# Performance work log

Measured on AMD Instinct MI355X. Metric: run time of the kernel, lower is better.

## Reference

```python
import jax, jax.numpy as jnp
import numpy as np

N, E, D = 50000, 800000, 128
EPS_BN = 1e-5   # torch BatchNorm1d default eps
EPS_AGG = 1e-6  # aggregation denominator eps


def setup_inputs() -> dict:
    key = jax.random.key(0)
    ks = jax.random.split(key, 20)
    s = 1.0 / np.sqrt(D)
    inp = {
        'h': jax.random.normal(ks[0], (N, D), jnp.float32),
        'e': jax.random.normal(ks[1], (E, D), jnp.float32),
    }
    for i, name in enumerate(['A1', 'A2', 'A3', 'B1', 'B2', 'B3']):
        inp['W_' + name] = (jax.random.normal(ks[2 + i], (D, D), jnp.float32) * s)
        inp['b_' + name] = (jax.random.normal(ks[8 + i], (D,), jnp.float32) * s)
    inp['gamma_e'] = jnp.ones((D,), jnp.float32)
    inp['beta_e'] = jnp.zeros((D,), jnp.float32)
    inp['gamma_h'] = jnp.ones((D,), jnp.float32)
    inp['beta_h'] = jnp.zeros((D,), jnp.float32)
    inp['src'] = jax.random.randint(ks[14], (E,), 0, N, dtype=jnp.int32)
    inp['dst'] = jax.random.randint(ks[15], (E,), 0, N, dtype=jnp.int32)
    return inp


def _bn(x, gamma, beta):
    # BatchNorm1d in training mode: biased batch statistics per channel
    mu = jnp.mean(x, axis=0)
    var = jnp.var(x, axis=0)
    return (x - mu) * jax.lax.rsqrt(var + EPS_BN) * gamma + beta


def reference(h, e, W_A1, b_A1, W_A2, b_A2, W_A3, b_A3,
              W_B1, b_B1, W_B2, b_B2, W_B3, b_B3,
              gamma_e, beta_e, gamma_h, beta_h, src, dst):
    n = h.shape[0]
    A1h = h @ W_A1 + b_A1
    A2h = h @ W_A2 + b_A2
    A3h = h @ W_A3 + b_A3
    B1h = h @ W_B1 + b_B1
    B2h = h @ W_B2 + b_B2
    B3e = e @ W_B3 + b_B3

    # Edge gate: e_ji (forward graph) == e_ik (reverse graph) by construction
    e_pre = B1h[src] + B2h[dst] + B3e            # [E, D]
    e_act = jax.nn.relu(_bn(e_pre, gamma_e, beta_e)) + e  # residual
    sigma = jax.nn.sigmoid(e_act)                # [E, D]

    seg = lambda v, idx: jax.ops.segment_sum(v, idx, num_segments=n)
    # forward aggregation at dst, backward aggregation (reverse graph) at src
    h_fwd = seg(sigma * A2h[src], dst) / (seg(sigma, dst) + EPS_AGG)
    h_bwd = seg(sigma * A3h[dst], src) / (seg(sigma, src) + EPS_AGG)

    h_new = A1h + h_fwd + h_bwd
    h_out = jax.nn.relu(_bn(h_new, gamma_h, beta_h)) + h  # residual; dropout p=0
    return h_out
```

## Files before the change

### kernel.cpp

```cpp
#include <hip/hip_runtime.h>
#include <hip/hip_bf16.h>

#define N_NODES 50000
#define N_EDGES 800000
#define D 128
#define NODE_TILES 3125
#define EDGE_TILES 50000

typedef __attribute__((ext_vector_type(4))) float f32x4;
typedef __attribute__((ext_vector_type(2))) float f32x2;
typedef __attribute__((ext_vector_type(8))) short bf16x8;

__device__ __forceinline__ unsigned short f2bf(float f) {
    __hip_bfloat16 h = __float2bfloat16(f);
    return __builtin_bit_cast(unsigned short, h);
}
__device__ __forceinline__ float bf2f(short s) {
    return __builtin_bit_cast(float, ((unsigned)(unsigned short)s) << 16);
}
__device__ __forceinline__ float bflo(unsigned u) { return __builtin_bit_cast(float, u << 16); }
__device__ __forceinline__ float bfhi(unsigned u) { return __builtin_bit_cast(float, u & 0xffff0000u); }

struct WPtrs   { const float* p[6]; };
struct NodeArgs{ const float* bias[3]; unsigned short* out[3]; int widx[3]; };


__global__ __launch_bounds__(256) void k_prep(WPtrs wp, unsigned short* __restrict__ wfrag) {
    int idx = blockIdx.x * 256 + threadIdx.x;
    if (idx >= 6 * 16384) return;
    int w  = idx >> 14;
    int r  = idx & 16383;
    int j  = r & 7;
    int l  = (r >> 3) & 63;
    int kc = r >> 9;
    int ki = kc >> 3, ct = kc & 7;
    int k  = ki * 32 + ((l >> 4) << 3) + j;
    int c  = ct * 16 + (l & 15);
    wfrag[idx] = f2bf(wp.p[w][k * D + c]);
}

__global__ __launch_bounds__(256) void k_node_gemm(const float* __restrict__ x,
                                                   const unsigned short* __restrict__ wfrag,
                                                   NodeArgs na, int ntiles) {
    __shared__ unsigned short ldsw[16384];
    const int z = blockIdx.z;
    {
        const uint4* sp = (const uint4*)(wfrag + (size_t)na.widx[z] * 16384);
        uint4* dp = (uint4*)ldsw;
        for (int i = threadIdx.x; i < 2048; i += 256) dp[i] = sp[i];
    }
    __syncthreads();
    const int lane = threadIdx.x & 63, wave = threadIdx.x >> 6;
    const int tile = blockIdx.x * 4 + wave;
    if (tile >= ntiles) return;
    const int lrow = lane & 15, lgrp = lane >> 4;

    const float* bias = na.bias[z];
    float bias_r[8];
#pragma unroll
    for (int ct = 0; ct < 8; ct++) bias_r[ct] = bias[ct * 16 + lrow];

    f32x4 acc[8];
#pragma unroll
    for (int ct = 0; ct < 8; ct++) acc[ct] = (f32x4)0.0f;

    const float* arow = x + (size_t)(tile * 16 + lrow) * D + lgrp * 8;
#pragma unroll
    for (int ki = 0; ki < 4; ki++) {
        f32x4 a0 = *(const f32x4*)(arow + ki * 32);
        f32x4 a1 = *(const f32x4*)(arow + ki * 32 + 4);
        bf16x8 af;
#pragma unroll
        for (int q = 0; q < 4; q++) { af[q] = (short)f2bf(a0[q]); af[q + 4] = (short)f2bf(a1[q]); }
#pragma unroll
        for (int ct = 0; ct < 8; ct++) {
            bf16x8 bf = *(const bf16x8*)(ldsw + ((ki * 8 + ct) * 64 + lane) * 8);
            acc[ct] = __builtin_amdgcn_mfma_f32_16x16x32_bf16(af, bf, acc[ct], 0, 0, 0);
        }
    }
    unsigned short* out16 = na.out[z];
#pragma unroll
    for (int j = 0; j < 4; j++) {
        bf16x8 pk;
#pragma unroll
        for (int ct = 0; ct < 8; ct++) pk[ct] = (short)f2bf(acc[ct][j] + bias_r[ct]);
        int rr = tile * 16 + lgrp * 4 + j;
        *(bf16x8*)(out16 + (size_t)rr * 128 + lrow * 8) = pk;
    }
}

__global__ __launch_bounds__(256) void k_hist(const int* __restrict__ src, const int* __restrict__ dst,
                                              int* __restrict__ cnt_f, int* __restrict__ cnt_b) {
    int e = blockIdx.x * 256 + threadIdx.x;
    if (e < N_EDGES) {
        atomicAdd(&cnt_f[dst[e]], 1);
        atomicAdd(&cnt_b[src[e]], 1);
    }
}

__global__ __launch_bounds__(1024) void k_scan(const int* __restrict__ cntf, int* __restrict__ offf,
                                               const int* __restrict__ cntb, int* __restrict__ offb) {
    const int* cnt = blockIdx.x ? cntb : cntf;
    int* off = blockIdx.x ? offb : offf;
    const int CH = 49;
    int t = threadIdx.x;
    int base = t * CH;
    int s = 0;
    for (int j = 0; j < CH; j++) { int i = base + j; s += (i < N_NODES) ? cnt[i] : 0; }
    __shared__ int tot[1024];
    tot[t] = s;
    __syncthreads();
    for (int d = 1; d < 1024; d <<= 1) {
        int v = (t >= d) ? tot[t - d] : 0;
        __syncthreads();
        tot[t] += v;
        __syncthreads();
    }
    int run = tot[t] - s;
    for (int j = 0; j < CH; j++) {
        int i = base + j;
        if (i < N_NODES) { run += cnt[i]; off[i + 1] = run; }
    }
    if (t == 0) off[0] = 0;
}

__global__ __launch_bounds__(256) void k_rank(const int* __restrict__ src, const int* __restrict__ dst,
                                              const int* __restrict__ off_f, const int* __restrict__ off_b,
                                              int* __restrict__ cnt2_f, int* __restrict__ cnt2_b,
                                              int2* __restrict__ idx_f, int2* __restrict__ idx_b) {
    int e = blockIdx.x * 256 + threadIdx.x;
    if (e < N_EDGES) {
        int d = dst[e], s = src[e];
        int rf = atomicAdd(&cnt2_f[d], 1);
        idx_f[off_f[d] + rf] = make_int2(e, s);
        int rb = atomicAdd(&cnt2_b[s], 1);
        idx_b[off_b[s] + rb] = make_int2(e, d);
    }
}

__global__ __launch_bounds__(256) void k_gather_stats(
        unsigned short* __restrict__ epre16,
        const unsigned short* __restrict__ B1p, const unsigned short* __restrict__ B2p,
        const int* __restrict__ src, const int* __restrict__ dst,
        float* __restrict__ ssum, float* __restrict__ sssq) {
    const int lane = threadIdx.x & 63, wave = threadIdx.x >> 6;
    const int t = lane & 15, sub = lane >> 4;
    float ss[8] = {0,0,0,0,0,0,0,0}, sq[8] = {0,0,0,0,0,0,0,0};
    const int NP = N_EDGES / 8;
    for (int q = blockIdx.x * 4 + wave; q < NP; q += gridDim.x * 4) {
        const int r0 = q * 8 + sub;
        const int r1 = r0 + 4;
        const int s0 = src[r0], d0 = dst[r0];
        const int s1 = src[r1], d1 = dst[r1];
        bf16x8 p0  = *(const bf16x8*)(epre16 + (((size_t)r0) << 7) + t * 8);
        bf16x8 p1  = *(const bf16x8*)(epre16 + (((size_t)r1) << 7) + t * 8);
        bf16x8 g1a = *(const bf16x8*)(B1p + (size_t)s0 * 128 + t * 8);
        bf16x8 g2a = *(const bf16x8*)(B2p + (size_t)d0 * 128 + t * 8);
        bf16x8 g1b = *(const bf16x8*)(B1p + (size_t)s1 * 128 + t * 8);
        bf16x8 g2b = *(const bf16x8*)(B2p + (size_t)d1 * 128 + t * 8);
        bf16x8 o0, o1;
#pragma unroll
        for (int ct = 0; ct < 8; ct++) {
            float v0 = bf2f(p0[ct]) + bf2f(g1a[ct]) + bf2f(g2a[ct]);
            float v1 = bf2f(p1[ct]) + bf2f(g1b[ct]) + bf2f(g2b[ct]);
            o0[ct] = (short)f2bf(v0);
            o1[ct] = (short)f2bf(v1);
            ss[ct] += v0 + v1; sq[ct] += v0 * v0 + v1 * v1;
        }
        *(bf16x8*)(epre16 + (((size_t)r0) << 7) + t * 8) = o0;
        *(bf16x8*)(epre16 + (((size_t)r1) << 7) + t * 8) = o1;
    }
#pragma unroll
    for (int ct = 0; ct < 8; ct++) {
        float a = ss[ct], b = sq[ct];
        a += __shfl_xor(a, 16); a += __shfl_xor(a, 32);
        b += __shfl_xor(b, 16); b += __shfl_xor(b, 32);
        if (lane < 16) {
            atomicAdd(&ssum[ct * 16 + lane], a);
            atomicAdd(&sssq[ct * 16 + lane], b);
        }
    }
}

__global__ void k_bnparam(const float* __restrict__ ssum, const float* __restrict__ sssq,
                          const float* __restrict__ gamma, const float* __restrict__ beta,
                          float cnt, float* __restrict__ scale, float* __restrict__ shift) {
    int c = threadIdx.x;
    float mu  = ssum[c] / cnt;
    float var = sssq[c] / cnt - mu * mu;
    float rs  = rsqrtf(var + 1e-5f);
    float sc  = rs * gamma[c];
    scale[c] = sc;
    shift[c] = beta[c] - mu * sc;
}

__global__ __launch_bounds__(256) void k_sigma(const float* __restrict__ e,
        const unsigned short* __restrict__ epre16, unsigned char* __restrict__ sigma,
        const float* __restrict__ scale_e, const float* __restrict__ shift_e) {
    const int lane = threadIdx.x & 63, wave = threadIdx.x >> 6;
    const int t = lane & 15, sub = lane >> 4;
    float sc[8], sh[8];
#pragma unroll
    for (int ct = 0; ct < 8; ct++) {
        int ch = ct * 16 + t;
        sc[ct] = scale_e[ch]; sh[ct] = shift_e[ch];
    }
    const int NQ = N_EDGES / 4;
    for (int q = blockIdx.x * 4 + wave; q < NQ; q += gridDim.x * 4) {
        const int r = q * 4 + sub;
        bf16x8 pk = *(const bf16x8*)(epre16 + (((size_t)r) << 7) + t * 8);
        const float* er = e + (size_t)r * 128 + t;
        float sg[8];
#pragma unroll
        for (int ct = 0; ct < 8; ct++) {
            float xn = bf2f(pk[ct]) * sc[ct] + sh[ct];
            float ea = fmaxf(xn, 0.0f) + er[ct * 16];
            sg[ct] = 1.0f / (1.0f + __expf(-ea));
        }
        int lo = 0, hi = 0;
        lo = __builtin_amdgcn_cvt_pk_fp8_f32(sg[0], sg[1], lo, false);
        lo = __builtin_amdgcn_cvt_pk_fp8_f32(sg[2], sg[3], lo, true);
        hi = __builtin_amdgcn_cvt_pk_fp8_f32(sg[4], sg[5], hi, false);
        hi = __builtin_amdgcn_cvt_pk_fp8_f32(sg[6], sg[7], hi, true);
        uint2 v; v.x = (unsigned)lo; v.y = (unsigned)hi;
        *(uint2*)(sigma + (size_t)r * 128 + t * 8) = v;
    }
}

__global__ __launch_bounds__(256) void k_aggregate(
        const unsigned char* __restrict__ sigma,
        const unsigned short* __restrict__ A1p, const unsigned short* __restrict__ A2p,
        const unsigned short* __restrict__ A3p,
        const int* __restrict__ off_f, const int2* __restrict__ idx_f,
        const int* __restrict__ off_b, const int2* __restrict__ idx_b,
        float* __restrict__ hnewp, float* __restrict__ ssum, float* __restrict__ sssq) {
    const int lane = threadIdx.x & 63, wave = threadIdx.x >> 6;
    const int wgl = blockIdx.x * 4 + wave;
    float ps0 = 0, pq0 = 0, ps1 = 0, pq1 = 0;
#pragma unroll 1
    for (int n = wgl * 4; n < wgl * 4 + 4; n++) {
        float fn0 = 0, fd0 = 0, fn1 = 0, fd1 = 0;
        float bn0 = 0, bd0 = 0, bn1 = 0, bd1 = 0;
        {
            int beg = off_f[n], end = off_f[n + 1];
            int i = beg;
            for (; i + 4 <= end; i += 4) {
                int2 e0 = idx_f[i], e1 = idx_f[i + 1], e2 = idx_f[i + 2], e3 = idx_f[i + 3];
                unsigned short w0 = *(const unsigned short*)(sigma + (size_t)e0.x * 128 + 2 * lane);
                unsigned short w1 = *(const unsigned short*)(sigma + (size_t)e1.x * 128 + 2 * lane);
                unsigned short w2 = *(const unsigned short*)(sigma + (size_t)e2.x * 128 + 2 * lane);
                unsigned short w3 = *(const unsigned short*)(sigma + (size_t)e3.x * 128 + 2 * lane);
                unsigned a0 = *(const unsigned*)(A2p + (size_t)e0.y * 128 + 2 * lane);
                unsigned a1 = *(const unsigned*)(A2p + (size_t)e1.y * 128 + 2 * lane);
                unsigned a2 = *(const unsigned*)(A2p + (size_t)e2.y * 128 + 2 * lane);
                unsigned a3 = *(const unsigned*)(A2p + (size_t)e3.y * 128 + 2 * lane);
                f32x2 s0 = __builtin_amdgcn_cvt_pk_f32_fp8((int)w0, false);
                f32x2 s1 = __builtin_amdgcn_cvt_pk_f32_fp8((int)w1, false);
                f32x2 s2 = __builtin_amdgcn_cvt_pk_f32_fp8((int)w2, false);
                f32x2 s3 = __builtin_amdgcn_cvt_pk_f32_fp8((int)w3, false);
                fn0 += s0.x * bflo(a0) + s1.x * bflo(a1) + s2.x * bflo(a2) + s3.x * bflo(a3);
                fd0 += s0.x + s1.x + s2.x + s3.x;
                fn1 += s0.y * bfhi(a0) + s1.y * bfhi(a1) + s2.y * bfhi(a2) + s3.y * bfhi(a3);
                fd1 += s0.y + s1.y + s2.y + s3.y;
            }
            for (; i < end; i++) {
                int2 e0 = idx_f[i];
                unsigned short w0 = *(const unsigned short*)(sigma + (size_t)e0.x * 128 + 2 * lane);
                unsigned a0 = *(const unsigned*)(A2p + (size_t)e0.y * 128 + 2 * lane);
                f32x2 s0 = __builtin_amdgcn_cvt_pk_f32_fp8((int)w0, false);
                fn0 += s0.x * bflo(a0); fd0 += s0.x;
                fn1 += s0.y * bfhi(a0); fd1 += s0.y;
            }
        }
        {
            int beg = off_b[n], end = off_b[n + 1];
            int i = beg;
            for (; i + 4 <= end; i += 4) {
                int2 e0 = idx_b[i], e1 = idx_b[i + 1], e2 = idx_b[i + 2], e3 = idx_b[i + 3];
                unsigned short w0 = *(const unsigned short*)(sigma + (size_t)e0.x * 128 + 2 * lane);
                unsigned short w1 = *(const unsigned short*)(sigma + (size_t)e1.x * 128 + 2 * lane);
                unsigned short w2 = *(const unsigned short*)(sigma + (size_t)e2.x * 128 + 2 * lane);
                unsigned short w3 = *(const unsigned short*)(sigma + (size_t)e3.x * 128 + 2 * lane);
                unsigned a0 = *(const unsigned*)(A3p + (size_t)e0.y * 128 + 2 * lane);
                unsigned a1 = *(const unsigned*)(A3p + (size_t)e1.y * 128 + 2 * lane);
                unsigned a2 = *(const unsigned*)(A3p + (size_t)e2.y * 128 + 2 * lane);
                unsigned a3 = *(const unsigned*)(A3p + (size_t)e3.y * 128 + 2 * lane);
                f32x2 s0 = __builtin_amdgcn_cvt_pk_f32_fp8((int)w0, false);
                f32x2 s1 = __builtin_amdgcn_cvt_pk_f32_fp8((int)w1, false);
                f32x2 s2 = __builtin_amdgcn_cvt_pk_f32_fp8((int)w2, false);
                f32x2 s3 = __builtin_amdgcn_cvt_pk_f32_fp8((int)w3, false);
                bn0 += s0.x * bflo(a0) + s1.x * bflo(a1) + s2.x * bflo(a2) + s3.x * bflo(a3);
                bd0 += s0.x + s1.x + s2.x + s3.x;
                bn1 += s0.y * bfhi(a0) + s1.y * bfhi(a1) + s2.y * bfhi(a2) + s3.y * bfhi(a3);
                bd1 += s0.y + s1.y + s2.y + s3.y;
            }
            for (; i < end; i++) {
                int2 e0 = idx_b[i];
                unsigned short w0 = *(const unsigned short*)(sigma + (size_t)e0.x * 128 + 2 * lane);
                unsigned a0 = *(const unsigned*)(A3p + (size_t)e0.y * 128 + 2 * lane);
                f32x2 s0 = __builtin_amdgcn_cvt_pk_f32_fp8((int)w0, false);
                bn0 += s0.x * bflo(a0); bd0 += s0.x;
                bn1 += s0.y * bfhi(a0); bd1 += s0.y;
            }
        }
        unsigned a1 = *(const unsigned*)(A1p + (size_t)n * 128 + 2 * lane);
        float hv0 = bflo(a1) + fn0 / (fd0 + 1e-6f) + bn0 / (bd0 + 1e-6f);
        float hv1 = bfhi(a1) + fn1 / (fd1 + 1e-6f) + bn1 / (bd1 + 1e-6f);
        f32x2 hv; hv.x = hv0; hv.y = hv1;
        *(f32x2*)(hnewp + (size_t)n * 128 + 2 * lane) = hv;
        ps0 += hv0; pq0 += hv0 * hv0;
        ps1 += hv1; pq1 += hv1 * hv1;
    }
    __shared__ float red[4][64][4];
    red[wave][lane][0] = ps0; red[wave][lane][1] = pq0;
    red[wave][lane][2] = ps1; red[wave][lane][3] = pq1;
    __syncthreads();
    if (threadIdx.x < 64) {
        int l = threadIdx.x;
        float s0 = 0, q0 = 0, s1 = 0, q1 = 0;
#pragma unroll
        for (int w = 0; w < 4; w++) {
            s0 += red[w][l][0]; q0 += red[w][l][1];
            s1 += red[w][l][2]; q1 += red[w][l][3];
        }
        int c0 = (((2 * l) & 7) << 4) + (l >> 2);
        atomicAdd(&ssum[c0], s0);      atomicAdd(&sssq[c0], q0);
        atomicAdd(&ssum[c0 + 16], s1); atomicAdd(&sssq[c0 + 16], q1);
    }
}

__global__ __launch_bounds__(256) void k_hout(const float* __restrict__ hnewp,
        const float* __restrict__ h, const float* __restrict__ scale,
        const float* __restrict__ shift, float* __restrict__ out) {
    __shared__ float sc[128], sh[128];
    if (threadIdx.x < 128) { sc[threadIdx.x] = scale[threadIdx.x]; sh[threadIdx.x] = shift[threadIdx.x]; }
    __syncthreads();
    const int total = N_NODES * 32;
    for (int i = blockIdx.x * blockDim.x + threadIdx.x; i < total; i += gridDim.x * blockDim.x) {
        int r = i >> 5, c4 = (i & 31) * 4;
        f32x4 hh = *(const f32x4*)(h + (size_t)r * 128 + c4);
        f32x4 o;
#pragma unroll
        for (int k = 0; k < 4; k++) {
            int ch = c4 + k;
            int p = (ch >> 4) + ((ch & 15) << 3);
            float v = hnewp[(size_t)r * 128 + p];
            o[k] = fmaxf(v * sc[ch] + sh[ch], 0.0f) + hh[k];
        }
        *(f32x4*)(out + (size_t)r * 128 + c4) = o;
    }
}

extern "C" void kernel_launch(void* const* d_in, const int* in_sizes, int n_in,
                              void* d_out, int out_size, void* d_ws, size_t ws_size,
                              hipStream_t stream) {
    const float* h = (const float*)d_in[0];
    const float* e = (const float*)d_in[1];
    const float* W[6] = {(const float*)d_in[2], (const float*)d_in[4], (const float*)d_in[6],
                         (const float*)d_in[8], (const float*)d_in[10], (const float*)d_in[12]};
    const float* b[6] = {(const float*)d_in[3], (const float*)d_in[5], (const float*)d_in[7],
                         (const float*)d_in[9], (const float*)d_in[11], (const float*)d_in[13]};
    const float* gamma_e = (const float*)d_in[14];
    const float* beta_e  = (const float*)d_in[15];
    const float* gamma_h = (const float*)d_in[16];
    const float* beta_h  = (const float*)d_in[17];
    const int* src = (const int*)d_in[18];
    const int* dst = (const int*)d_in[19];
    float* out = (float*)d_out;

    char* ws = (char*)d_ws;
    unsigned short* wfrag = (unsigned short*)(ws);
    float* scale_e = (float*)(ws + 196608);
    float* shift_e = (float*)(ws + 197120);
    float* scale_h = (float*)(ws + 197632);
    float* shift_h = (float*)(ws + 198144);
    float* ssum_e  = (float*)(ws + 198656);
    float* sssq_e  = (float*)(ws + 199168);
    float* ssum_h  = (float*)(ws + 199680);
    float* sssq_h  = (float*)(ws + 200192);
    int*   cnt_f   = (int*)(ws + 200704);
    int*   cnt_b   = (int*)(ws + 400704);
    int*   cnt2_f  = (int*)(ws + 600704);
    int*   cnt2_b  = (int*)(ws + 800704);
    int*   off_f   = (int*)(ws + 1000704);
    int*   off_b   = (int*)(ws + 1200768);
    unsigned short* slot0 = (unsigned short*)(ws + 1400832);
    unsigned short* slot1 = slot0 + 6400000;
    unsigned short* slot2 = slot1 + 6400000;
    unsigned char* sigma = (unsigned char*)(ws + 39800832);
    int2*  idx_f   = (int2*)(ws + 142200832);
    int2*  idx_b   = idx_f + N_EDGES;
    float* hnewp   = (float*)(ws + 155000832);
    unsigned short* epre16 = (unsigned short*)(ws + 180600832);

    hipMemsetAsync(ws + 198656, 0, 802048, stream);

    WPtrs wp;
    for (int i = 0; i < 6; i++) wp.p[i] = W[i];
    k_prep<<<384, 256, 0, stream>>>(wp, wfrag);

    NodeArgs nb;
    nb.bias[0] = b[3]; nb.bias[1] = b[4]; nb.bias[2] = b[4];
    nb.out[0] = slot0; nb.out[1] = slot1; nb.out[2] = slot1;
    nb.widx[0] = 3;    nb.widx[1] = 4;    nb.widx[2] = 4;
    k_node_gemm<<<dim3(782, 1, 2), 256, 0, stream>>>(h, wfrag, nb, NODE_TILES);

    k_hist<<<3125, 256, 0, stream>>>(src, dst, cnt_f, cnt_b);
    k_scan<<<2, 1024, 0, stream>>>(cnt_f, off_f, cnt_b, off_b);
    k_rank<<<3125, 256, 0, stream>>>(src, dst, off_f, off_b, cnt2_f, cnt2_b, idx_f, idx_b);

    NodeArgs ne;
    ne.bias[0] = b[5]; ne.bias[1] = b[5]; ne.bias[2] = b[5];
    ne.out[0] = epre16; ne.out[1] = epre16; ne.out[2] = epre16;
    ne.widx[0] = 5;    ne.widx[1] = 5;    ne.widx[2] = 5;
    k_node_gemm<<<dim3(12500, 1, 1), 256, 0, stream>>>(e, wfrag, ne, EDGE_TILES);

    k_gather_stats<<<2048, 256, 0, stream>>>(epre16, slot0, slot1, src, dst, ssum_e, sssq_e);
    k_bnparam<<<1, 128, 0, stream>>>(ssum_e, sssq_e, gamma_e, beta_e, (float)N_EDGES, scale_e, shift_e);
    k_sigma<<<2048, 256, 0, stream>>>(e, epre16, sigma, scale_e, shift_e);

    NodeArgs na;
    na.bias[0] = b[0]; na.bias[1] = b[1]; na.bias[2] = b[2];
    na.out[0] = slot0; na.out[1] = slot1; na.out[2] = slot2;
    na.widx[0] = 0;    na.widx[1] = 1;    na.widx[2] = 2;
    k_node_gemm<<<dim3(782, 1, 3), 256, 0, stream>>>(h, wfrag, na, NODE_TILES);

    k_aggregate<<<3125, 256, 0, stream>>>(sigma, slot0, slot1, slot2,
                                          off_f, idx_f, off_b, idx_b, hnewp, ssum_h, sssq_h);
    k_bnparam<<<1, 128, 0, stream>>>(ssum_h, sssq_h, gamma_h, beta_h, (float)N_NODES, scale_h, shift_h);
    k_hout<<<1024, 256, 0, stream>>>(hnewp, h, scale_h, shift_h, out);
}
```

Measured before the change: 996.8 us.

## Drop e_pre writeback; recompute gathered B1/B2 sum in sigma kernel

```diff
diff --git a/kernel.cpp b/kernel.cpp
--- a/kernel.cpp
+++ b/kernel.cpp
@@ -138,37 +138,34 @@
     }
 }
 
-__global__ __launch_bounds__(256) void k_gather_stats(
-        unsigned short* __restrict__ epre16,
+__global__ __launch_bounds__(256) void k_stats(
+        const unsigned short* __restrict__ epre16,
         const unsigned short* __restrict__ B1p, const unsigned short* __restrict__ B2p,
         const int* __restrict__ src, const int* __restrict__ dst,
         float* __restrict__ ssum, float* __restrict__ sssq) {
     const int lane = threadIdx.x & 63, wave = threadIdx.x >> 6;
     const int t = lane & 15, sub = lane >> 4;
     float ss[8] = {0,0,0,0,0,0,0,0}, sq[8] = {0,0,0,0,0,0,0,0};
-    const int NP = N_EDGES / 8;
-    for (int q = blockIdx.x * 4 + wave; q < NP; q += gridDim.x * 4) {
-        const int r0 = q * 8 + sub;
-        const int r1 = r0 + 4;
-        const int s0 = src[r0], d0 = dst[r0];
-        const int s1 = src[r1], d1 = dst[r1];
-        bf16x8 p0  = *(const bf16x8*)(epre16 + (((size_t)r0) << 7) + t * 8);
-        bf16x8 p1  = *(const bf16x8*)(epre16 + (((size_t)r1) << 7) + t * 8);
-        bf16x8 g1a = *(const bf16x8*)(B1p + (size_t)s0 * 128 + t * 8);
-        bf16x8 g2a = *(const bf16x8*)(B2p + (size_t)d0 * 128 + t * 8);
-        bf16x8 g1b = *(const bf16x8*)(B1p + (size_t)s1 * 128 + t * 8);
-        bf16x8 g2b = *(const bf16x8*)(B2p + (size_t)d1 * 128 + t * 8);
-        bf16x8 o0, o1;
-#pragma unroll
-        for (int ct = 0; ct < 8; ct++) {
-            float v0 = bf2f(p0[ct]) + bf2f(g1a[ct]) + bf2f(g2a[ct]);
-            float v1 = bf2f(p1[ct]) + bf2f(g1b[ct]) + bf2f(g2b[ct]);
-            o0[ct] = (short)f2bf(v0);
-            o1[ct] = (short)f2bf(v1);
-            ss[ct] += v0 + v1; sq[ct] += v0 * v0 + v1 * v1;
-        }
-        *(bf16x8*)(epre16 + (((size_t)r0) << 7) + t * 8) = o0;
-        *(bf16x8*)(epre16 + (((size_t)r1) << 7) + t * 8) = o1;
+    const int NG = N_EDGES / 16;
+    for (int q = blockIdx.x * 4 + wave; q < NG; q += gridDim.x * 4) {
+        const int rb = q * 16 + sub;
+        int s4[4], d4[4];
+#pragma unroll
+        for (int u = 0; u < 4; u++) { s4[u] = src[rb + u * 4]; d4[u] = dst[rb + u * 4]; }
+        bf16x8 p[4], g1[4], g2[4];
+#pragma unroll
+        for (int u = 0; u < 4; u++) p[u]  = *(const bf16x8*)(epre16 + (((size_t)(rb + u * 4)) << 7) + t * 8);
+#pragma unroll
+        for (int u = 0; u < 4; u++) g1[u] = *(const bf16x8*)(B1p + (size_t)s4[u] * 128 + t * 8);
+#pragma unroll
+        for (int u = 0; u < 4; u++) g2[u] = *(const bf16x8*)(B2p + (size_t)d4[u] * 128 + t * 8);
+#pragma unroll
+        for (int u = 0; u < 4; u++)
+#pragma unroll
+            for (int ct = 0; ct < 8; ct++) {
+                float v = bf2f(p[u][ct]) + bf2f(g1[u][ct]) + bf2f(g2[u][ct]);
+                ss[ct] += v; sq[ct] += v * v;
+            }
     }
 #pragma unroll
     for (int ct = 0; ct < 8; ct++) {
@@ -195,7 +192,10 @@
 }
 
 __global__ __launch_bounds__(256) void k_sigma(const float* __restrict__ e,
-        const unsigned short* __restrict__ epre16, unsigned char* __restrict__ sigma,
+        const unsigned short* __restrict__ epre16,
+        const unsigned short* __restrict__ B1p, const unsigned short* __restrict__ B2p,
+        const int* __restrict__ src, const int* __restrict__ dst,
+        unsigned char* __restrict__ sigma,
         const float* __restrict__ scale_e, const float* __restrict__ shift_e) {
     const int lane = threadIdx.x & 63, wave = threadIdx.x >> 6;
     const int t = lane & 15, sub = lane >> 4;
@@ -208,12 +208,16 @@
     const int NQ = N_EDGES / 4;
     for (int q = blockIdx.x * 4 + wave; q < NQ; q += gridDim.x * 4) {
         const int r = q * 4 + sub;
+        const int s = src[r], d = dst[r];
         bf16x8 pk = *(const bf16x8*)(epre16 + (((size_t)r) << 7) + t * 8);
+        bf16x8 g1 = *(const bf16x8*)(B1p + (size_t)s * 128 + t * 8);
+        bf16x8 g2 = *(const bf16x8*)(B2p + (size_t)d * 128 + t * 8);
         const float* er = e + (size_t)r * 128 + t;
         float sg[8];
 #pragma unroll
         for (int ct = 0; ct < 8; ct++) {
-            float xn = bf2f(pk[ct]) * sc[ct] + sh[ct];
+            float v  = bf2f(pk[ct]) + bf2f(g1[ct]) + bf2f(g2[ct]);
+            float xn = v * sc[ct] + sh[ct];
             float ea = fmaxf(xn, 0.0f) + er[ct * 16];
             sg[ct] = 1.0f / (1.0f + __expf(-ea));
         }
@@ -415,9 +419,9 @@
     ne.widx[0] = 5;    ne.widx[1] = 5;    ne.widx[2] = 5;
     k_node_gemm<<<dim3(12500, 1, 1), 256, 0, stream>>>(e, wfrag, ne, EDGE_TILES);
 
-    k_gather_stats<<<2048, 256, 0, stream>>>(epre16, slot0, slot1, src, dst, ssum_e, sssq_e);
+    k_stats<<<2048, 256, 0, stream>>>(epre16, slot0, slot1, src, dst, ssum_e, sssq_e);
     k_bnparam<<<1, 128, 0, stream>>>(ssum_e, sssq_e, gamma_e, beta_e, (float)N_EDGES, scale_e, shift_e);
-    k_sigma<<<2048, 256, 0, stream>>>(e, epre16, sigma, scale_e, shift_e);
+    k_sigma<<<2048, 256, 0, stream>>>(e, epre16, slot0, slot1, src, dst, sigma, scale_e, shift_e);
 
     NodeArgs na;
     na.bias[0] = b[0]; na.bias[1] = b[1]; na.bias[2] = b[2];
```

New measurement: 1.007 ms. Within noise of the previous version (+1.0%).
